# Kernel tuning notes

Hardware: AMD Instinct MI355X
Metric: run time of the kernel (lower is better)

The kernel has to match this reference:

```python
import jax, jax.numpy as jnp
import numpy as np

T, B, D, N, REL, OUT = 16, 128, 96, 8, 96, 64  # time, batch, slot_size, num_slot, rel_size, out_att_size
EPS = 1e-5


def setup_inputs() -> dict:
    key = jax.random.key(0)
    ks = jax.random.split(key, 12)
    rn = lambda k, shape, s: jax.random.normal(k, shape, dtype=jnp.float32) * s
    stdev_i = 1.0 / np.sqrt(2.0 * D)
    stdev_r = 1.0 / np.sqrt(2.0 * D + N)
    return {
        'x': jax.random.normal(ks[0], (T, B, D), dtype=jnp.float32),
        'Wqkv': rn(ks[1], (D, 3 * N), 0.1), 'bqkv': jnp.zeros((3 * N,), jnp.float32),
        'ln_g': jnp.ones((D, 3 * N), jnp.float32), 'ln_b': jnp.zeros((D, 3 * N), jnp.float32),
        'a1': rn(ks[2], (), 0.1), 'a2': rn(ks[3], (), 0.1), 'a3': rn(ks[4], (), 0.1),
        'W2': rn(ks[5], (N * D, D), 0.03), 'b2': jnp.zeros((D,), jnp.float32),
        'Wr': rn(ks[6], (D * D, REL), 0.01), 'br': jnp.zeros((REL,), jnp.float32),
        'W3': rn(ks[7], (N * REL, OUT), 0.03), 'b3': jnp.zeros((OUT,), jnp.float32),
        'item_bias': jax.random.uniform(ks[8], (D, D), jnp.float32, -stdev_i, stdev_i),
        'rel_bias': jax.random.uniform(ks[9], (N, D, D), jnp.float32, -stdev_r, stdev_r),
    }


def reference(x, Wqkv, bqkv, ln_g, ln_b, a1, a2, a3, W2, b2, Wr, br, W3, b3, item_bias, rel_bias):
    Bb = x.shape[1]
    Mi0 = jnp.broadcast_to(item_bias, (Bb, D, D))
    rel0 = jnp.broadcast_to(rel_bias, (Bb, N, D, D))
    W2r = W2.reshape(N, D, D)  # rel_projector2 weight, rows indexed by flattened (n, d)

    def step(carry, xt):  # xt: [B, D]
        Mi, rel = carry
        Mi = Mi + xt[:, :, None] * xt[:, None, :]                     # Mi + outer(x, x)
        Vtr = jnp.einsum('bdf,bndf->bf', Mi, rel)                     # [B, D]
        X2 = Vtr[:, :, None] * xt[:, None, :]                         # [B, D, D]
        qkv = (Mi + a2 * X2) @ Wqkv + bqkv                            # [B, D, 3N]
        mu = qkv.mean(axis=(1, 2), keepdims=True)                     # LayerNorm over [D, 3N]
        var = qkv.var(axis=(1, 2), keepdims=True)
        qkv = (qkv - mu) * jax.lax.rsqrt(var + EPS) * ln_g + ln_b
        qkv = qkv.transpose(0, 2, 1)                                  # [B, 3N, D]
        q, k, v = qkv[:, :N], qkv[:, N:2 * N], qkv[:, 2 * N:]
        # op_att: out[b,i] = sum_j outer(tanh(q_i * k_j), v_j)
        t = jnp.tanh(q[:, :, None, :] * k[:, None, :, :])             # [B, N, N, D]
        R0 = jnp.einsum('bijd,bje->bide', t, v)                       # [B, N, D, D]
        rel = a1 * rel + R0
        R2 = jnp.einsum('bnde,ndf->bef', R0, W2r) + b2                # [B, D, D]
        Mi = Mi + a3 * R2
        r_vec = (rel.reshape(Bb, N, D * D) @ Wr + br).reshape(Bb, N * REL)
        out = r_vec @ W3 + b3                                          # [B, OUT]
        return (Mi, rel), out

    (_, _), hx = jax.lax.scan(step, (Mi0, rel0), x)
    return hx  # [T, B, OUT]
```

## Files before the change

### kernel.cpp

```cpp
#include <hip/hip_runtime.h>
#include <math.h>

#define T_ 16
#define B_ 128
#define C3 24
#define OUT_ 64
#define EPS_ 1e-5f

typedef __attribute__((ext_vector_type(8))) short bf16x8;
typedef __attribute__((ext_vector_type(4))) float f32x4;
typedef __attribute__((ext_vector_type(4))) unsigned uint32x4;

union FragU { unsigned u[4]; bf16x8 f; };

__device__ __forceinline__ short f2bf(float x) {
    unsigned u = __float_as_uint(x);
    return (short)((u + 0x7fffu + ((u >> 16) & 1u)) >> 16);
}
__device__ __forceinline__ void splitf(float x, short& h, short& l) {
    unsigned u = __float_as_uint(x);
    unsigned hb = (u + 0x7fffu + ((u >> 16) & 1u)) & 0xffff0000u;
    float res = x - __uint_as_float(hb);
    unsigned v = __float_as_uint(res);
    h = (short)(hb >> 16);
    l = (short)((v + 0x7fffu + ((v >> 16) & 1u)) >> 16);
}
__device__ __forceinline__ f32x4 mfma16(bf16x8 a, bf16x8 b, f32x4 c) {
    return __builtin_amdgcn_mfma_f32_16x16x32_bf16(a, b, c, 0, 0, 0);
}
__device__ __forceinline__ f32x4 mfma16v(bf16x8 a, bf16x8 b, f32x4 c) {
    f32x4 d;
    asm("s_nop 1\n\tv_mfma_f32_16x16x32_bf16 %0, %1, %2, %3"
        : "=v"(d)
        : "v"(a), "v"(b), "0"(c));
    return d;
}
#define MFMA_FENCE3(a0, a1, a2) \
    asm volatile("s_nop 7\n\ts_nop 7" : "+v"(a0), "+v"(a1), "+v"(a2))

__device__ __forceinline__ float fast_tanh(float z) {
    float a = fminf(fabsf(z), 9.0f);
    float e = __expf(2.0f * a);
    float t = 1.0f - 2.0f / (e + 1.0f);
    return copysignf(t, z);
}

__global__ __launch_bounds__(768, 1) void prep_mega(
    const float* __restrict__ Wr, const float* __restrict__ W2, const float* __restrict__ W3,
    const float* __restrict__ rel_bias,
    short* __restrict__ WrBH, short* __restrict__ WrBL,
    short* __restrict__ W2H, short* __restrict__ W2L,
    short* __restrict__ W3H, short* __restrict__ W3L,
    float* __restrict__ y0)
{
    __shared__ __attribute__((aligned(16))) char ps[37248];
    const int bid = blockIdx.x, tid = threadIdx.x;
    if (bid < 96) {
        float* s_wr = (float*)ps;
        const int d = bid;
        for (int q2 = tid; q2 < 9216; q2 += 768) {
            int e2 = q2 / 96, r2 = q2 % 96;
            s_wr[e2 * 97 + r2] = Wr[(size_t)d * 9216 + q2];
        }
        __syncthreads();
#pragma unroll
        for (int s = 0; s < 12; ++s) {
            int q = tid + 768 * s;
            int jj = q & 7, lane = (q >> 3) & 63, f2 = q >> 9;
            int kf = f2 % 3, rt = f2 / 3;
            int col = lane & 15, grp = lane >> 4;
            int e = kf * 32 + grp * 8 + jj;
            int r = rt * 16 + col;
            short h, l; splitf(s_wr[e * 97 + r], h, l);
            size_t oidx = (size_t)d * 9216 + q;
            WrBH[oidx] = h; WrBL[oidx] = l;
        }
    } else if (bid < 120) {
        float* s_w2 = (float*)ps;
        const int kb = bid - 96;
        for (int q2 = tid; q2 < 3072; q2 += 768) {
            int rr = q2 / 96, ff = q2 % 96;
            s_w2[rr * 97 + ff] = W2[(size_t)((rr >> 2) * 96 + 4 * kb + (rr & 3)) * 96 + ff];
        }
        __syncthreads();
#pragma unroll
        for (int s = 0; s < 4; ++s) {
            int q = tid + 768 * s;
            int jj = q & 7, lane = (q >> 3) & 63, rt = q >> 9;
            int col = lane & 15, grp = lane >> 4;
            short h, l; splitf(s_w2[(jj * 4 + grp) * 97 + rt * 16 + col], h, l);
            size_t oidx = (size_t)512 * kb + (q & 511) + (size_t)12288 * rt;
            W2H[oidx] = h; W2L[oidx] = l;
        }
    } else if (bid < 144) {
        float* s_w3 = (float*)ps;
        const int kb = bid - 120;
        for (int q2 = tid; q2 < 2048; q2 += 768) {
            int kl = q2 >> 6, oo = q2 & 63;
            s_w3[kl * 65 + oo] = W3[(size_t)kb * 2048 + q2];
        }
        __syncthreads();
        for (int q = tid; q < 2048; q += 768) {
            int jj = q & 7, lane = (q >> 3) & 63, ot = q >> 9;
            int col = lane & 15, grp = lane >> 4;
            short h, l; splitf(s_w3[(grp * 8 + jj) * 65 + ot * 16 + col], h, l);
            size_t oidx = (size_t)512 * kb + (q & 511) + (size_t)12288 * ot;
            W3H[oidx] = h; W3L[oidx] = l;
        }
    } else {
        float* s = (float*)ps;
        const int blk = bid - 144;
        const int n = blk >> 3, sl = blk & 7;
        const int r = tid % 96, p = tid / 96;
        const float* rb = rel_bias + n * 9216 + sl * 1152;
        float acc = 0.f;
        for (int i = p * 144; i < p * 144 + 144; ++i)
            acc += rb[i] * Wr[(size_t)(sl * 1152 + i) * 96 + r];
        s[tid] = acc;
        __syncthreads();
        if (tid < 96) {
            float tot = 0.f;
            for (int q = 0; q < 8; ++q) tot += s[q * 96 + tid];
            atomicAdd(&y0[n * 96 + tid], tot);
        }
    }
}

__global__ __attribute__((amdgpu_flat_work_group_size(768, 768), amdgpu_waves_per_eu(3, 3)))
void stm_rec(
    const float* __restrict__ x, const float* __restrict__ Wqkv, const float* __restrict__ bqkv,
    const float* __restrict__ ln_g, const float* __restrict__ ln_b,
    const float* __restrict__ a1p, const float* __restrict__ a2p, const float* __restrict__ a3p,
    const float* __restrict__ b2,
    const float* __restrict__ item_bias, const float* __restrict__ rel_bias,
    const short* __restrict__ W2H, const short* __restrict__ W2L,
    short* __restrict__ t2g, short* __restrict__ vgb)
{
    __shared__ __attribute__((aligned(16))) char smem[143424];
    const int tid = threadIdx.x;
    const int b = blockIdx.x;
    const int wv = tid >> 6, lane = tid & 63, col = lane & 15, grp = lane >> 4;
    const float a1 = a1p[0], a2 = a2p[0], a3 = a3p[0];

    float* s_xall    = (float*)(smem);
    float* s_scr     = (float*)(smem + 6144);
    float* s_scrB    = (float*)(smem + 15744);
    float* s_Wq      = (float*)(smem + 18816);
    float* s_lng     = (float*)(smem + 28032);
    float* s_lnb     = (float*)(smem + 37632);
    float* s_tsum    = (float*)(smem + 47232);
    float* s_v       = (float*)(smem + 50304);
    float* s_G0      = (float*)(smem + 53376);
    float* s_G1      = (float*)(smem + 56448);
    float* s_xtWqAll = (float*)(smem + 59520);
    float* s_b2Wq    = (float*)(smem + 61056);
    float* s_bq      = (float*)(smem + 61152);
    float* s_b2v     = (float*)(smem + 61248);
    float* s_red     = (float*)(smem + 61632);
    short* s_tH      = (short*)(smem + 61760);
    short* s_tL      = (short*)(smem + 74176);
    short* s_t2L     = (short*)(smem + 86592);
    float* s_vp      = (float*)(smem + 98880);
    float* s_rS      = (float*)(smem + 103488);

    const int de = tid >> 3, ef0 = (tid & 7) * 12;
    const int t13 = tid * 13;
    float rMi[12], rQ[3];
#pragma unroll
    for (int ii = 0; ii < 12; ++ii) {
        int idx = de * 96 + ef0 + ii;
        rMi[ii] = item_bias[idx];
        float ss = 0.f;
        for (int n = 0; n < 8; ++n) ss += rel_bias[n * 9216 + idx];
        s_rS[t13 + ii] = ss;
    }

    for (int i = tid; i < 1536; i += 768)
        s_xall[i] = x[((size_t)(i / 96) * B_ + b) * 96 + (i % 96)];
    for (int i = tid; i < 2304; i += 768) {
        int dd = i / 24, cc = i % 24;
        s_Wq[i] = Wqkv[i];
        s_lng[dd * 25 + cc] = ln_g[i];
        s_lnb[dd * 25 + cc] = ln_b[i];
    }
    if (tid < 24) s_bq[tid] = bqkv[tid];
    if (tid < 96) s_b2v[tid] = b2[tid];
    __syncthreads();
#pragma unroll
    for (int pp = 0; pp < 3; ++pp) {
        int o = tid + 768 * pp; int i = o / C3, c = o % C3;
        float acc = 0.f;
        const float* ib = item_bias + i * 96;
        for (int k = 0; k < 96; ++k) acc += ib[k] * s_Wq[k * C3 + c];
        rQ[pp] = acc;
    }
    { int c = tid % C3, p = tid / C3; float acc = 0.f;
      for (int k = 3 * p; k < 3 * p + 3; ++k) acc += s_b2v[k] * s_Wq[k * C3 + c];
      s_scr[p * 25 + c] = acc; }
    if (tid < 384) {
        int t = tid / 24, c = tid % 24;
        float acc = 0.f;
        const float* xr = s_xall + t * 96;
        for (int k = 0; k < 96; ++k) acc += xr[k] * s_Wq[k * C3 + c];
        s_xtWqAll[tid] = acc;
    }
    __syncthreads();
    if (tid < C3) { float a = 0.f; for (int p = 0; p < 32; ++p) a += s_scr[p * 25 + tid]; s_b2Wq[tid] = a; }
    __syncthreads();

    for (int t = 0; t < T_; ++t) {
        const float* xt = s_xall + t * 96;
        const float* xtWq = s_xtWqAll + t * 24;
        {
            float xde = xt[de];
            const float4* xp = (const float4*)&xt[ef0];
            float4 x0 = xp[0], x1 = xp[1], x2 = xp[2];
            rMi[0] += xde * x0.x; rMi[1] += xde * x0.y; rMi[2] += xde * x0.z; rMi[3] += xde * x0.w;
            rMi[4] += xde * x1.x; rMi[5] += xde * x1.y; rMi[6] += xde * x1.z; rMi[7] += xde * x1.w;
            rMi[8] += xde * x2.x; rMi[9] += xde * x2.y; rMi[10] += xde * x2.z; rMi[11] += xde * x2.w;
        }
        {
            float p12[12];
#pragma unroll
            for (int ii = 0; ii < 12; ++ii) p12[ii] = rMi[ii] * s_rS[t13 + ii];
#pragma unroll
            for (int ii = 0; ii < 12; ++ii) {
                p12[ii] += __shfl_xor(p12[ii], 8);
                p12[ii] += __shfl_xor(p12[ii], 16);
                p12[ii] += __shfl_xor(p12[ii], 32);
            }
            if ((lane >> 3) == 0) {
#pragma unroll
                for (int ii = 0; ii < 12; ++ii)
                    s_vp[wv * 96 + (lane & 7) * 12 + ii] = p12[ii];
            }
        }
        __syncthreads();
        if (t > 0) {
#pragma unroll
            for (int pp = 0; pp < 3; ++pp) {
                int o = tid + 768 * pp; int i = o / C3, c = o % C3;
                float a = s_b2Wq[c];
#pragma unroll
                for (int j = 0; j < 8; ++j) {
                    float g = s_scrB[j * C3 + c] + s_scrB[192 + j * C3 + c]
                            + s_scrB[384 + j * C3 + c] + s_scrB[576 + j * C3 + c];
                    a += s_v[j * 96 + i] * g;
                }
                rQ[pp] += a3 * a;
            }
        }
        {
            const int i0 = tid / 24, c = tid % 24;
            float ls = 0.f, lq = 0.f;
#pragma unroll
            for (int pp = 0; pp < 3; ++pp) {
                const int i = i0 + 32 * pp;
                float vtr = 0.f;
#pragma unroll
                for (int w = 0; w < 12; ++w) vtr += s_vp[w * 96 + i];
                rQ[pp] += xt[i] * xtWq[c];
                float qv = rQ[pp] + a2 * vtr * xtWq[c] + s_bq[c];
                s_scr[i * 25 + c] = qv;
                ls += qv; lq += qv * qv;
            }
            for (int off = 32; off > 0; off >>= 1) { ls += __shfl_down(ls, off); lq += __shfl_down(lq, off); }
            if (lane == 0) { s_red[wv] = ls; s_red[16 + wv] = lq; }
        }
        __syncthreads();
        {
            float S = 0.f, Qs = 0.f;
            for (int w = 0; w < 12; ++w) { S += s_red[w]; Qs += s_red[16 + w]; }
            const float mu = S * (1.0f / 2304.f);
            const float rstd = rsqrtf(Qs * (1.0f / 2304.f) - mu * mu + EPS_);
            const int j = tid / 96, d = tid % 96;
            const int d25 = d * 25;
            {
                int o = d25 + 16 + j;
                float vv = (s_scr[o] - mu) * rstd * s_lng[o] + s_lnb[o];
                s_v[tid] = vv;
                __builtin_nontemporal_store(f2bf(vv), &vgb[((size_t)(t * B_ + b)) * 768 + tid]);
            }
            int ok = d25 + 8 + j;
            float kk = (s_scr[ok] - mu) * rstd * s_lng[ok] + s_lnb[ok];
            float tv0, tv1;
            unsigned hp0, hp1, hp2, hp3, lp0, lp1, lp2, lp3;
            float ts = 0.f;
#pragma unroll
            for (int q = 0; q < 4; ++q) {
                int oq0 = d25 + 2 * q, oq1 = oq0 + 1;
                float q0 = (s_scr[oq0] - mu) * rstd * s_lng[oq0] + s_lnb[oq0];
                float q1 = (s_scr[oq1] - mu) * rstd * s_lng[oq1] + s_lnb[oq1];
                tv0 = fast_tanh(q0 * kk);
                tv1 = fast_tanh(q1 * kk);
                ts += tv0 + tv1;
                short h0, l0, h1, l1;
                splitf(tv0, h0, l0); splitf(tv1, h1, l1);
                unsigned hh = (unsigned)(unsigned short)h0 | ((unsigned)(unsigned short)h1 << 16);
                unsigned ll = (unsigned)(unsigned short)l0 | ((unsigned)(unsigned short)l1 << 16);
                if (q == 0) { hp0 = hh; lp0 = ll; }
                else if (q == 1) { hp1 = hh; lp1 = ll; }
                else if (q == 2) { hp2 = hh; lp2 = ll; }
                else { hp3 = hh; lp3 = ll; }
                s_t2L[(2 * q) * 768 + d * 8 + j] = h0;
                s_t2L[(2 * q + 1) * 768 + d * 8 + j] = h1;
            }
            *(uint4*)&s_tH[j * 776 + d * 8] = make_uint4(hp0, hp1, hp2, hp3);
            *(uint4*)&s_tL[j * 776 + d * 8] = make_uint4(lp0, lp1, lp2, lp3);
            s_tsum[j * 96 + d] = ts;
        }
        __syncthreads();
        {
            uint32x4 tv = *(const uint32x4*)&s_t2L[tid * 8];
            __builtin_nontemporal_store(tv,
                (uint32x4*)&t2g[((size_t)(t * B_ + b)) * 6144 + tid * 8]);
        }
        {
            const int rt = wv % 6, kh = wv / 6;
            f32x4 aHH = {0,0,0,0}, aLH = {0,0,0,0}, aHL = {0,0,0,0};
#pragma unroll 4
            for (int s2 = 0; s2 < 12; ++s2) {
                int kb = kh * 12 + s2;
                bf16x8 ah = {}; bf16x8 al = {};
                if (col < 8) {
                    ah = *(const bf16x8*)&s_tH[col * 776 + kb * 32 + grp * 8];
                    al = *(const bf16x8*)&s_tL[col * 776 + kb * 32 + grp * 8];
                }
                int fo = ((rt * 24 + kb) * 64 + lane) * 8;
                bf16x8 bh = *(const bf16x8*)&W2H[fo];
                bf16x8 bl = *(const bf16x8*)&W2L[fo];
                aHH = mfma16v(ah, bh, aHH);
                aLH = mfma16v(al, bh, aLH);
                aHL = mfma16v(ah, bl, aHL);
            }
            MFMA_FENCE3(aHH, aLH, aHL);
            f32x4 accG;
#pragma unroll
            for (int reg = 0; reg < 4; ++reg) accG[reg] = (aHH[reg] + aLH[reg]) + aHL[reg];
            float* dst = (kh == 0) ? s_G0 : s_G1;
            if (grp < 2) {
#pragma unroll
                for (int reg = 0; reg < 4; ++reg)
                    dst[(grp * 4 + reg) * 96 + rt * 16 + col] = accG[reg];
            }
        }
        __syncthreads();
        { int oo = tid % 192, q = tid / 192; int jg = oo / C3, cc = oo % C3;
          float a = 0.f;
          for (int f = q * 24; f < q * 24 + 24; ++f)
              a += (s_G0[jg * 96 + f] + s_G1[jg * 96 + f]) * s_Wq[f * C3 + cc];
          s_scrB[tid] = a; }
        {
            float sn[12];
#pragma unroll
            for (int ii = 0; ii < 12; ++ii) sn[ii] = 0.f;
#pragma unroll
            for (int j = 0; j < 8; ++j) {
                const float tj = s_tsum[j * 96 + de];
                const float4* vp = (const float4*)&s_v[j * 96 + ef0];
#pragma unroll
                for (int q4 = 0; q4 < 3; ++q4) {
                    float4 vv = vp[q4];
                    sn[q4*4+0] += tj*vv.x; sn[q4*4+1] += tj*vv.y;
                    sn[q4*4+2] += tj*vv.z; sn[q4*4+3] += tj*vv.w;
                }
            }
#pragma unroll
            for (int ii = 0; ii < 12; ++ii)
                s_rS[t13 + ii] = a1 * s_rS[t13 + ii] + sn[ii];
        }
        {
            float r2[12];
#pragma unroll
            for (int ii = 0; ii < 12; ++ii) r2[ii] = 0.f;
#pragma unroll
            for (int j = 0; j < 8; ++j) {
                const float vj = s_v[j * 96 + de];
                const float4* g0 = (const float4*)&s_G0[j * 96 + ef0];
                const float4* g1 = (const float4*)&s_G1[j * 96 + ef0];
#pragma unroll
                for (int q4 = 0; q4 < 3; ++q4) {
                    float4 ga = g0[q4], gb = g1[q4];
                    r2[q4*4+0] += vj*(ga.x+gb.x); r2[q4*4+1] += vj*(ga.y+gb.y);
                    r2[q4*4+2] += vj*(ga.z+gb.z); r2[q4*4+3] += vj*(ga.w+gb.w);
                }
            }
#pragma unroll
            for (int ii = 0; ii < 12; ++ii)
                rMi[ii] += a3 * (r2[ii] + s_b2v[ef0 + ii]);
        }
    }
}

__global__ __launch_bounds__(384, 2) void stm_tail(
    const short* __restrict__ WrBH, const short* __restrict__ WrBL,
    const short* __restrict__ W3H, const short* __restrict__ W3L,
    const short* __restrict__ t2g, const short* __restrict__ vgb,
    const float* __restrict__ y0, const float* __restrict__ br,
    const float* __restrict__ W3f, const float* __restrict__ b3,
    float* __restrict__ zg, float* __restrict__ c0v, float* __restrict__ cbrv)
{
    __shared__ __attribute__((aligned(16))) short sPT[6 * 5120];
    short* DyH = sPT;
    short* DyL = sPT + 6208;

    const int tid = threadIdx.x;

    if (blockIdx.x >= 256) {
        float* red = (float*)sPT;
        const int o = tid & 63, seg = tid >> 6;
        if (blockIdx.x == 256) {
            float pa = 0.f;
            for (int i = seg * 128; i < seg * 128 + 128; ++i)
                pa += y0[i] * W3f[(size_t)i * 64 + o];
            red[seg * 64 + o] = pa;
            __syncthreads();
            if (tid < 64) {
                float s = 0.f;
                for (int q = 0; q < 6; ++q) s += red[q * 64 + tid];
                c0v[tid] = s;
            }
        } else {
            float pb = 0.f;
            for (int i = seg * 128; i < seg * 128 + 128; ++i)
                pb += br[i % 96] * W3f[(size_t)i * 64 + o];
            red[seg * 64 + o] = pb;
            __syncthreads();
            if (tid < 64) {
                float s = b3[tid];
                for (int q = 0; q < 6; ++q) s += red[q * 64 + tid];
                cbrv[tid] = s;
            }
        }
        return;
    }

    const int b = blockIdx.x & 127, tg = blockIdx.x >> 7;
    const int wv6 = tid >> 6, lane = tid & 63, col = lane & 15, grp = lane >> 4;
    const int rt6 = wv6;
    const int th = tg * 8;
    short* PTw = sPT + wv6 * 5120;

    bf16x8 Av[4][3];
#pragma unroll
    for (int p = 0; p < 4; ++p)
#pragma unroll
        for (int kf = 0; kf < 3; ++kf) {
            int t = th + 2 * p + (col >> 3);
            int j = col & 7;
            uint4 z = *(const uint4*)&vgb[((size_t)(t * B_ + b)) * 768 + j * 96 + kf * 32 + grp * 8];
            FragU F; F.u[0] = z.x; F.u[1] = z.y; F.u[2] = z.z; F.u[3] = z.w;
            Av[p][kf] = F.f;
        }
    f32x4 accD[8];
#pragma unroll
    for (int btl = 0; btl < 8; ++btl) accD[btl] = (f32x4){0.f, 0.f, 0.f, 0.f};

    FragU A2r[8];
    bf16x8 bhA[3], blA[3], bhB[3], blB[3];
#pragma unroll
    for (int kf = 0; kf < 3; ++kf) {
        const int fo = ((0 * 18 + rt6 * 3 + kf) * 64 + lane) * 8;
        bhA[kf] = *(const bf16x8*)&WrBH[fo];
        blA[kf] = *(const bf16x8*)&WrBL[fo];
    }

#define TAIL_BODY(DL, CH, CL, NH, NL)                                          \
    {                                                                          \
        const int d = g4 * 4 + (DL);                                           \
        if ((DL) < 3 || g4 < 23) {                                             \
            const int dn = d + 1;                                              \
            _Pragma("unroll")                                                  \
            for (int kf = 0; kf < 3; ++kf) {                                   \
                const int fo = ((dn * 18 + rt6 * 3 + kf) * 64 + lane) * 8;     \
                NH[kf] = *(const bf16x8*)&WrBH[fo];                            \
                NL[kf] = *(const bf16x8*)&WrBL[fo];                            \
            }                                                                  \
        }                                                                      \
        if ((DL) == 1) {                                                       \
            _Pragma("unroll")                                                  \
            for (int btl = 0; btl < 8; ++btl) {                                \
                A2r[btl].u[0] = 0; A2r[btl].u[1] = 0;                          \
                A2r[btl].u[2] = 0; A2r[btl].u[3] = 0;                          \
                if (col < 8) {                                                 \
                    const int tt = th + btl;                                   \
                    uint4 z = *(const uint4*)&t2g[((size_t)(tt * B_ + b)) * 6144 \
                              + col * 768 + g4 * 32 + grp * 8];                \
                    A2r[btl].u[0] = z.x; A2r[btl].u[1] = z.y;                  \
                    A2r[btl].u[2] = z.z; A2r[btl].u[3] = z.w;                  \
                }                                                              \
            }                                                                  \
        }                                                                      \
        f32x4 aPv[4];                                                          \
        _Pragma("unroll")                                                      \
        for (int p = 0; p < 4; ++p) aPv[p] = (f32x4){0.f, 0.f, 0.f, 0.f};      \
        _Pragma("unroll")                                                      \
        for (int kf = 0; kf < 3; ++kf) {                                       \
            _Pragma("unroll")                                                  \
            for (int p = 0; p < 4; ++p) aPv[p] = mfma16(Av[p][kf], CH[kf], aPv[p]); \
            _Pragma("unroll")                                                  \
            for (int p = 0; p < 4; ++p) aPv[p] = mfma16(Av[p][kf], CL[kf], aPv[p]); \
        }                                                                      \
        {                                                                      \
            const int j0 = (grp & 1) * 4;                                      \
            const int bo = grp >> 1;                                           \
            _Pragma("unroll")                                                  \
            for (int p = 0; p < 4; ++p) {                                      \
                const int btl = 2 * p + bo;                                    \
                uint2 uu;                                                      \
                uu.x = (unsigned)(unsigned short)f2bf(aPv[p][0]) |             \
                       ((unsigned)(unsigned short)f2bf(aPv[p][1]) << 16);      \
                uu.y = (unsigned)(unsigned short)f2bf(aPv[p][2]) |             \
                       ((unsigned)(unsigned short)f2bf(aPv[p][3]) << 16);      \
                *(uint2*)&PTw[btl * 640 + col * 40 + (DL) * 8 + j0] = uu;      \
            }                                                                  \
        }                                                                      \
        if ((DL) == 3) {                                                       \
            _Pragma("unroll")                                                  \
            for (int btl = 0; btl < 8; ++btl) {                                \
                bf16x8 B2 = *(const bf16x8*)&PTw[btl * 640 + col * 40 + grp * 8]; \
                accD[btl] = mfma16(A2r[btl].f, B2, accD[btl]);                 \
            }                                                                  \
        }                                                                      \
    }

    for (int g4 = 0; g4 < 24; ++g4) {
        TAIL_BODY(0, bhA, blA, bhB, blB)
        TAIL_BODY(1, bhB, blB, bhA, blA)
        TAIL_BODY(2, bhA, blA, bhB, blB)
        TAIL_BODY(3, bhB, blB, bhA, blA)
    }
#undef TAIL_BODY

    __syncthreads();
    if (grp < 2) {
#pragma unroll
        for (int btl = 0; btl < 8; ++btl)
#pragma unroll
            for (int reg = 0; reg < 4; ++reg) {
                short h, l; splitf(accD[btl][reg], h, l);
                int idx = btl * 776 + (grp * 4 + reg) * 96 + rt6 * 16 + col;
                DyH[idx] = h; DyL[idx] = l;
            }
    }
    __syncthreads();
    if (wv6 < 4) {
        const int ot = wv6;
        f32x4 zHH = {0,0,0,0}, zLH = {0,0,0,0}, zHL = {0,0,0,0};
#pragma unroll 4
        for (int kb = 0; kb < 24; ++kb) {
            bf16x8 ah = {}; bf16x8 al = {};
            if (col < 8) {
                ah = *(const bf16x8*)&DyH[col * 776 + kb * 32 + grp * 8];
                al = *(const bf16x8*)&DyL[col * 776 + kb * 32 + grp * 8];
            }
            int fo = ((ot * 24 + kb) * 64 + lane) * 8;
            bf16x8 bhw = *(const bf16x8*)&W3H[fo];
            bf16x8 blw = *(const bf16x8*)&W3L[fo];
            zHH = mfma16(ah, bhw, zHH);
            zLH = mfma16(al, bhw, zLH);
            zHL = mfma16(ah, blw, zHL);
        }
        if (grp < 2) {
#pragma unroll
            for (int reg = 0; reg < 4; ++reg) {
                int tl = grp * 4 + reg;
                zg[((size_t)(b * 16 + th + tl)) * 64 + ot * 16 + col] = zHH[reg] + zLH[reg] + zHL[reg];
            }
        }
    }
}

__global__ __launch_bounds__(64) void stm_fin(
    const float* __restrict__ a1p, const float* __restrict__ zg,
    const float* __restrict__ c0v, const float* __restrict__ cbrv,
    float* __restrict__ out)
{
    const int tid = threadIdx.x, b = blockIdx.x;
    const float a1 = a1p[0];
    float u = c0v[tid];
    const float cbr = cbrv[tid];
    for (int t = 0; t < T_; ++t) {
        u = a1 * u + zg[((size_t)(b * 16 + t)) * 64 + tid];
        out[((size_t)(t * B_ + b)) * OUT_ + tid] = u + cbr;
    }
}

extern "C" void kernel_launch(void* const* d_in, const int* in_sizes, int n_in,
                              void* d_out, int out_size, void* d_ws, size_t ws_size,
                              hipStream_t stream) {
    const float* x         = (const float*)d_in[0];
    const float* Wqkv      = (const float*)d_in[1];
    const float* bqkv      = (const float*)d_in[2];
    const float* ln_g      = (const float*)d_in[3];
    const float* ln_b      = (const float*)d_in[4];
    const float* a1        = (const float*)d_in[5];
    const float* a2        = (const float*)d_in[6];
    const float* a3        = (const float*)d_in[7];
    const float* W2        = (const float*)d_in[8];
    const float* b2        = (const float*)d_in[9];
    const float* Wr        = (const float*)d_in[10];
    const float* br        = (const float*)d_in[11];
    const float* W3        = (const float*)d_in[12];
    const float* b3        = (const float*)d_in[13];
    const float* item_bias = (const float*)d_in[14];
    const float* rel_bias  = (const float*)d_in[15];
    float* out = (float*)d_out;

    char* ws = (char*)d_ws;
    short* WrBH = (short*)ws;
    short* WrBL = (short*)(ws + 1769472);
    short* W2H  = (short*)(ws + 3538944);
    short* W2L  = (short*)(ws + 3686400);
    short* W3H  = (short*)(ws + 3833856);
    short* W3L  = (short*)(ws + 3932160);
    float* y0   = (float*)(ws + 4030464);
    short* t2g  = (short*)(ws + 4034048);
    short* vgb  = (short*)(ws + 29199872);
    float* zg   = (float*)(ws + 32345600);
    float* c0v  = (float*)(ws + 32869888);
    float* cbrv = (float*)(ws + 32870144);

    hipMemsetAsync(y0, 0, 3072, stream);
    hipLaunchKernelGGL(prep_mega, dim3(208), dim3(768), 0, stream,
                       Wr, W2, W3, rel_bias, WrBH, WrBL, W2H, W2L, W3H, W3L, y0);
    hipLaunchKernelGGL(stm_rec, dim3(B_), dim3(768), 0, stream,
                       x, Wqkv, bqkv, ln_g, ln_b, a1, a2, a3,
                       b2, item_bias, rel_bias, W2H, W2L, t2g, vgb);
    hipLaunchKernelGGL(stm_tail, dim3(258), dim3(384), 0, stream,
                       WrBH, WrBL, W3H, W3L, t2g, vgb,
                       y0, br, W3, b3, zg, c0v, cbrv);
    hipLaunchKernelGGL(stm_fin, dim3(B_), dim3(64), 0, stream,
                       a1, zg, c0v, cbrv, out);
}
```

Baseline: 459.5 us.

## Move Mi state from registers to LDS and store t2 directly to global

The per-thread 12-element Mi accumulator moves out of registers into a padded LDS array next to the relation-sum state, which lowers register pressure in the recurrent kernel. The t2 tile no longer goes through an LDS staging buffer with a separate 16-byte vector store after a barrier. Each thread now writes its bf16 values straight to global memory as scattered 2-byte nontemporal stores, and the packed LDS writes are split into 4-byte stores. The cost is more LDS traffic per step, finer-grained global stores, and an extra barrier at the end of each time step.

```diff
diff --git a/kernel.cpp b/kernel.cpp
--- a/kernel.cpp
+++ b/kernel.cpp
@@ -9,7 +9,6 @@
 
 typedef __attribute__((ext_vector_type(8))) short bf16x8;
 typedef __attribute__((ext_vector_type(4))) float f32x4;
-typedef __attribute__((ext_vector_type(4))) unsigned uint32x4;
 
 union FragU { unsigned u[4]; bf16x8 f; };
 
@@ -136,7 +135,7 @@
     const short* __restrict__ W2H, const short* __restrict__ W2L,
     short* __restrict__ t2g, short* __restrict__ vgb)
 {
-    __shared__ __attribute__((aligned(16))) char smem[143424];
+    __shared__ __attribute__((aligned(16))) char smem[161088];
     const int tid = threadIdx.x;
     const int b = blockIdx.x;
     const int wv = tid >> 6, lane = tid & 63, col = lane & 15, grp = lane >> 4;
@@ -159,20 +158,20 @@
     float* s_red     = (float*)(smem + 61632);
     short* s_tH      = (short*)(smem + 61760);
     short* s_tL      = (short*)(smem + 74176);
-    short* s_t2L     = (short*)(smem + 86592);
-    float* s_vp      = (float*)(smem + 98880);
-    float* s_rS      = (float*)(smem + 103488);
+    float* s_Mi      = (float*)(smem + 86592);
+    float* s_S       = (float*)(smem + 123840);
+    float* s_vp      = (float*)(smem + 53376);
 
     const int de = tid >> 3, ef0 = (tid & 7) * 12;
-    const int t13 = tid * 13;
-    float rMi[12], rQ[3];
+    const int miBase = de * 97 + ef0;
+    float rQ[3];
 #pragma unroll
     for (int ii = 0; ii < 12; ++ii) {
         int idx = de * 96 + ef0 + ii;
-        rMi[ii] = item_bias[idx];
+        s_Mi[miBase + ii] = item_bias[idx];
         float ss = 0.f;
         for (int n = 0; n < 8; ++n) ss += rel_bias[n * 9216 + idx];
-        s_rS[t13 + ii] = ss;
+        s_S[miBase + ii] = ss;
     }
 
     for (int i = tid; i < 1536; i += 768)
@@ -215,14 +214,16 @@
             float xde = xt[de];
             const float4* xp = (const float4*)&xt[ef0];
             float4 x0 = xp[0], x1 = xp[1], x2 = xp[2];
-            rMi[0] += xde * x0.x; rMi[1] += xde * x0.y; rMi[2] += xde * x0.z; rMi[3] += xde * x0.w;
-            rMi[4] += xde * x1.x; rMi[5] += xde * x1.y; rMi[6] += xde * x1.z; rMi[7] += xde * x1.w;
-            rMi[8] += xde * x2.x; rMi[9] += xde * x2.y; rMi[10] += xde * x2.z; rMi[11] += xde * x2.w;
-        }
-        {
+            float xv[12] = { x0.x, x0.y, x0.z, x0.w,
+                             x1.x, x1.y, x1.z, x1.w,
+                             x2.x, x2.y, x2.z, x2.w };
             float p12[12];
 #pragma unroll
-            for (int ii = 0; ii < 12; ++ii) p12[ii] = rMi[ii] * s_rS[t13 + ii];
+            for (int ii = 0; ii < 12; ++ii) {
+                float m = s_Mi[miBase + ii] + xde * xv[ii];
+                s_Mi[miBase + ii] = m;
+                p12[ii] = m * s_S[miBase + ii];
+            }
 #pragma unroll
             for (int ii = 0; ii < 12; ++ii) {
                 p12[ii] += __shfl_xor(p12[ii], 8);
@@ -283,38 +284,29 @@
             }
             int ok = d25 + 8 + j;
             float kk = (s_scr[ok] - mu) * rstd * s_lng[ok] + s_lnb[ok];
-            float tv0, tv1;
-            unsigned hp0, hp1, hp2, hp3, lp0, lp1, lp2, lp3;
+            const size_t tb2 = ((size_t)(t * B_ + b)) * 6144 + d * 8 + j;
             float ts = 0.f;
+            const int tb = j * 776 + d * 8;
 #pragma unroll
             for (int q = 0; q < 4; ++q) {
                 int oq0 = d25 + 2 * q, oq1 = oq0 + 1;
                 float q0 = (s_scr[oq0] - mu) * rstd * s_lng[oq0] + s_lnb[oq0];
                 float q1 = (s_scr[oq1] - mu) * rstd * s_lng[oq1] + s_lnb[oq1];
-                tv0 = fast_tanh(q0 * kk);
-                tv1 = fast_tanh(q1 * kk);
+                float tv0 = fast_tanh(q0 * kk);
+                float tv1 = fast_tanh(q1 * kk);
                 ts += tv0 + tv1;
                 short h0, l0, h1, l1;
                 splitf(tv0, h0, l0); splitf(tv1, h1, l1);
-                unsigned hh = (unsigned)(unsigned short)h0 | ((unsigned)(unsigned short)h1 << 16);
-                unsigned ll = (unsigned)(unsigned short)l0 | ((unsigned)(unsigned short)l1 << 16);
-                if (q == 0) { hp0 = hh; lp0 = ll; }
-                else if (q == 1) { hp1 = hh; lp1 = ll; }
-                else if (q == 2) { hp2 = hh; lp2 = ll; }
-                else { hp3 = hh; lp3 = ll; }
-                s_t2L[(2 * q) * 768 + d * 8 + j] = h0;
-                s_t2L[(2 * q + 1) * 768 + d * 8 + j] = h1;
-            }
-            *(uint4*)&s_tH[j * 776 + d * 8] = make_uint4(hp0, hp1, hp2, hp3);
-            *(uint4*)&s_tL[j * 776 + d * 8] = make_uint4(lp0, lp1, lp2, lp3);
+                *(unsigned*)&s_tH[tb + 2 * q] =
+                    (unsigned)(unsigned short)h0 | ((unsigned)(unsigned short)h1 << 16);
+                *(unsigned*)&s_tL[tb + 2 * q] =
+                    (unsigned)(unsigned short)l0 | ((unsigned)(unsigned short)l1 << 16);
+                __builtin_nontemporal_store(h0, &t2g[tb2 + (size_t)(2 * q) * 768]);
+                __builtin_nontemporal_store(h1, &t2g[tb2 + (size_t)(2 * q + 1) * 768]);
+            }
             s_tsum[j * 96 + d] = ts;
         }
         __syncthreads();
-        {
-            uint32x4 tv = *(const uint32x4*)&s_t2L[tid * 8];
-            __builtin_nontemporal_store(tv,
-                (uint32x4*)&t2g[((size_t)(t * B_ + b)) * 6144 + tid * 8]);
-        }
         {
             const int rt = wv % 6, kh = wv / 6;
             f32x4 aHH = {0,0,0,0}, aLH = {0,0,0,0}, aHL = {0,0,0,0};
@@ -367,7 +359,7 @@
             }
 #pragma unroll
             for (int ii = 0; ii < 12; ++ii)
-                s_rS[t13 + ii] = a1 * s_rS[t13 + ii] + sn[ii];
+                s_S[miBase + ii] = a1 * s_S[miBase + ii] + sn[ii];
         }
         {
             float r2[12];
@@ -387,8 +379,9 @@
             }
 #pragma unroll
             for (int ii = 0; ii < 12; ++ii)
-                rMi[ii] += a3 * (r2[ii] + s_b2v[ef0 + ii]);
-        }
+                s_Mi[miBase + ii] += a3 * (r2[ii] + s_b2v[ef0 + ii]);
+        }
+        __syncthreads();
     }
 }
 
```

Result: slower. 499.1 us (+8.6%).
